# Kernel optimization log

Hardware: AMD Instinct MI355X
Metric: run time of the kernel (lower is better)

Reference implementation:

```python
import jax, jax.numpy as jnp
import numpy as np
import math

NUM_HEADS = 16


def setup_inputs() -> dict:
    key = jax.random.key(0)
    ks = jax.random.split(key, 5)
    B, C, H = 2, 2048, 1024
    return {
        "x": jax.random.normal(ks[0], (B, C, H), dtype=jnp.float32),
        "Wqkv_w": jax.random.normal(ks[1], (3 * H, H), dtype=jnp.float32) * (1.0 / math.sqrt(H)),
        "Wqkv_b": jax.random.normal(ks[2], (3 * H,), dtype=jnp.float32) * 0.02,
        "Wo_w": jax.random.normal(ks[3], (H, H), dtype=jnp.float32) * (1.0 / math.sqrt(H)),
        "Wo_b": jax.random.normal(ks[4], (H,), dtype=jnp.float32) * 0.02,
    }


def reference(x, Wqkv_w, Wqkv_b, Wo_w, Wo_b):
    B, C, H = x.shape
    nh = NUM_HEADS
    hd = H // nh
    # QKV projection (torch Linear: x @ W.T + b)
    qkv = x @ Wqkv_w.T + Wqkv_b                      # [B, C, 3H]
    qkv = qkv.reshape(B, C, 3, nh, hd)
    qkv = jnp.transpose(qkv, (2, 0, 3, 1, 4))        # [3, B, nh, C, hd]
    q, k, v = qkv[0], qkv[1], qkv[2]
    scale = 1.0 / math.sqrt(hd)
    att = jnp.einsum('bhqd,bhkd->bhqk', q, k) * scale  # [B, nh, C, C]
    causal = jnp.triu(jnp.ones((C, C), dtype=bool), k=1)  # True above diagonal
    att = jnp.where(causal[None, None], jnp.float32(-jnp.inf), att)
    att = jax.nn.softmax(att, axis=-1)
    # dropout p set to 0 (eval-mode math)
    out = jnp.einsum('bhqk,bhkd->bhqd', att, v)       # [B, nh, C, hd]
    out = jnp.transpose(out, (0, 2, 1, 3)).reshape(B, C, H)
    return out @ Wo_w.T + Wo_b
```

## Files before the change

### kernel.cpp

```cpp
#include <hip/hip_runtime.h>
#include <hip/hip_bf16.h>
#include <math.h>

typedef unsigned short u16;
typedef __attribute__((ext_vector_type(8))) __bf16 bf16x8;
typedef __attribute__((ext_vector_type(4))) float f32x4;
typedef __attribute__((ext_vector_type(8))) unsigned short u16x8;
typedef __attribute__((ext_vector_type(4))) unsigned int u32x4;

__device__ __forceinline__ u16 f2bf(float f) {
  union { float f; unsigned u; } x; x.f = f;
  unsigned r = x.u + 0x7fffu + ((x.u >> 16) & 1u);
  return (u16)(r >> 16);
}

__device__ __forceinline__ void gload16(const u16* g, u16* l) {
  __builtin_amdgcn_global_load_lds(
      (const __attribute__((address_space(1))) void*)g,
      (__attribute__((address_space(3))) void*)l, 16, 0, 0);
}

#define MFMA16(a, b, c) __builtin_amdgcn_mfma_f32_16x16x32_bf16((a), (b), (c), 0, 0, 0)

__global__ __launch_bounds__(256) void cast_bf16_kernel(
    const float* __restrict__ in, u16* __restrict__ out, int n4) {
  int i = blockIdx.x * 256 + threadIdx.x;
  if (i >= n4) return;
  f32x4 v = *(const f32x4*)(in + (size_t)i * 4);
  u16 o0 = f2bf(v[0]), o1 = f2bf(v[1]), o2 = f2bf(v[2]), o3 = f2bf(v[3]);
  unsigned lo = (unsigned)o0 | ((unsigned)o1 << 16);
  unsigned hi = (unsigned)o2 | ((unsigned)o3 << 16);
  ((unsigned*)out)[(size_t)i * 2] = lo;
  ((unsigned*)out)[(size_t)i * 2 + 1] = hi;
}

__device__ __forceinline__ void gemm_bt_128(
    const u16* __restrict__ A, const u16* __restrict__ B, int K, int m0, int n0,
    u16* As, u16* Bs, f32x4 acc[4][4]) {
  const int tid = threadIdx.x;
  const int lane = tid & 63;
  const int wr = tid >> 7;
  const int wc = (tid >> 6) & 1;
  for (int k0 = 0; k0 < K; k0 += 64) {
    #pragma unroll
    for (int it = 0; it < 4; ++it) {
      int c = it * 256 + tid;
      int row = c >> 3;
      int ko = (c & 7) << 3;
      gload16(A + (size_t)(m0 + row) * K + (k0 + ko), As + c * 8);
      gload16(B + (size_t)(n0 + row) * K + (k0 + ko), Bs + c * 8);
    }
    __syncthreads();
    #pragma unroll
    for (int kk = 0; kk < 2; ++kk) {
      bf16x8 a[4], b[4];
      #pragma unroll
      for (int m = 0; m < 4; ++m)
        a[m] = *(const bf16x8*)(As + ((wr * 64 + m * 16 + (lane & 15)) * 64 +
                                      kk * 32 + ((lane >> 4) << 3)));
      #pragma unroll
      for (int n = 0; n < 4; ++n)
        b[n] = *(const bf16x8*)(Bs + ((wc * 64 + n * 16 + (lane & 15)) * 64 +
                                      kk * 32 + ((lane >> 4) << 3)));
      #pragma unroll
      for (int m = 0; m < 4; ++m)
        #pragma unroll
        for (int n = 0; n < 4; ++n)
          acc[m][n] = MFMA16(a[m], b[n], acc[m][n]);
    }
    __syncthreads();
  }
}

__global__ __launch_bounds__(256) void gemm_qkv_kernel(
    const u16* __restrict__ X, const u16* __restrict__ W, const float* __restrict__ bias,
    u16* __restrict__ Qb, u16* __restrict__ Kb, u16* __restrict__ Vb) {
  __shared__ __align__(16) u16 As[128 * 64];
  __shared__ __align__(16) u16 Bs[128 * 64];
  f32x4 acc[4][4];
  #pragma unroll
  for (int m = 0; m < 4; ++m)
    #pragma unroll
    for (int n = 0; n < 4; ++n) acc[m][n] = (f32x4){0.f, 0.f, 0.f, 0.f};
  const int m0 = blockIdx.y * 128;
  const int n0 = blockIdx.x * 128;
  gemm_bt_128(X, W, 1024, m0, n0, As, Bs, acc);
  const int lane = threadIdx.x & 63;
  const int wr = threadIdx.x >> 7, wc = (threadIdx.x >> 6) & 1;
  #pragma unroll
  for (int m = 0; m < 4; ++m) {
    #pragma unroll
    for (int n = 0; n < 4; ++n) {
      #pragma unroll
      for (int j = 0; j < 4; ++j) {
        int row = m0 + wr * 64 + m * 16 + ((lane >> 4) << 2) + j;
        int col = n0 + wc * 64 + n * 16 + (lane & 15);
        float v = acc[m][n][j] + bias[col];
        int which = col >> 10;
        int rem = col & 1023;
        int h = rem >> 6, d = rem & 63;
        int bb = row >> 11, q = row & 2047;
        if (which == 0) v *= 0.125f;
        u16* dst = (which == 0) ? Qb : (which == 1 ? Kb : Vb);
        dst[((size_t)((bb * 16 + h) * 2048 + q)) * 64 + d] = f2bf(v);
      }
    }
  }
}

__global__ __launch_bounds__(256) void gemm_out_kernel(
    const u16* __restrict__ Ain, const u16* __restrict__ W, const float* __restrict__ bias,
    float* __restrict__ out) {
  __shared__ __align__(16) u16 As[128 * 64];
  __shared__ __align__(16) u16 Bs[128 * 64];
  f32x4 acc[4][4];
  #pragma unroll
  for (int m = 0; m < 4; ++m)
    #pragma unroll
    for (int n = 0; n < 4; ++n) acc[m][n] = (f32x4){0.f, 0.f, 0.f, 0.f};
  const int m0 = blockIdx.y * 128;
  const int n0 = blockIdx.x * 128;
  gemm_bt_128(Ain, W, 1024, m0, n0, As, Bs, acc);
  const int lane = threadIdx.x & 63;
  const int wr = threadIdx.x >> 7, wc = (threadIdx.x >> 6) & 1;
  #pragma unroll
  for (int m = 0; m < 4; ++m) {
    #pragma unroll
    for (int n = 0; n < 4; ++n) {
      #pragma unroll
      for (int j = 0; j < 4; ++j) {
        int row = m0 + wr * 64 + m * 16 + ((lane >> 4) << 2) + j;
        int col = n0 + wc * 64 + n * 16 + (lane & 15);
        out[(size_t)row * 1024 + col] = acc[m][n][j] + bias[col];
      }
    }
  }
}

__device__ __forceinline__ void attn_one(
    const u16* __restrict__ Qh, const u16* __restrict__ Kh, const u16* __restrict__ Vh,
    u16* __restrict__ Ob, int bb, int h, int qt,
    u16 (*Ks)[64 * 64], u16 (*Vt)[64 * 64]) {
  const int tid = threadIdx.x, lane = tid & 63, w = tid >> 6;
  const int g = lane >> 4, q15 = lane & 15;

  bf16x8 qf[2];
  const int qrow = qt * 64 + w * 16 + q15;
  #pragma unroll
  for (int kk = 0; kk < 2; ++kk)
    qf[kk] = *(const bf16x8*)(Qh + (size_t)qrow * 64 + kk * 32 + g * 8);

  f32x4 acc_o[4];
  #pragma unroll
  for (int n = 0; n < 4; ++n) acc_o[n] = (f32x4){0.f, 0.f, 0.f, 0.f};
  float m_run = -INFINITY, l_run = 0.f;

  const int nt = qt + 1;

  auto stageK = [&](int t, int buf) {
    #pragma unroll
    for (int it = 0; it < 2; ++it) {
      int c = it * 256 + tid;
      int row = c >> 3, b8 = c & 7;
      gload16(Kh + (size_t)(t * 64 + row) * 64 + ((b8 ^ (row & 7)) << 3),
              Ks[buf] + c * 8);
    }
  };

  stageK(0, 0);
  #pragma unroll
  for (int it = 0; it < 2; ++it) {
    int kloc = it * 32 + (tid >> 3);
    int d0 = (tid & 7) << 3;
    u16x8 v = *(const u16x8*)(Vh + (size_t)kloc * 64 + d0);
    #pragma unroll
    for (int i = 0; i < 8; ++i) {
      int d = d0 + i;
      int fv = (d + (d >> 3)) & 7;
      Vt[0][d * 64 + (((kloc >> 3) ^ fv) << 3) + (kloc & 7)] = v[i];
    }
  }
  __syncthreads();

  for (int t = 0; t < nt; ++t) {
    const int cur = t & 1;
    const bool pre = (t + 1 < nt);
    u16x8 vreg[2];
    if (pre) {
      stageK(t + 1, cur ^ 1);
      #pragma unroll
      for (int it = 0; it < 2; ++it) {
        int kloc = it * 32 + (tid >> 3);
        int d0 = (tid & 7) << 3;
        vreg[it] = *(const u16x8*)(Vh + (size_t)((t + 1) * 64 + kloc) * 64 + d0);
      }
    }

    f32x4 accs[4];
    __builtin_amdgcn_s_setprio(1);
    #pragma unroll
    for (int cb = 0; cb < 4; ++cb) {
      accs[cb] = (f32x4){0.f, 0.f, 0.f, 0.f};
      #pragma unroll
      for (int kk = 0; kk < 2; ++kk) {
        int row = cb * 16 + q15;
        int kblk = kk * 4 + g;
        bf16x8 kf = *(const bf16x8*)(Ks[cur] + row * 64 + ((kblk ^ (row & 7)) << 3));
        accs[cb] = MFMA16(kf, qf[kk], accs[cb]);
      }
    }
    __builtin_amdgcn_s_setprio(0);
    if (t == nt - 1) {
      #pragma unroll
      for (int cb = 0; cb < 4; ++cb)
        #pragma unroll
        for (int j = 0; j < 4; ++j) {
          int kg = t * 64 + cb * 16 + 4 * g + j;
          int qg = qt * 64 + w * 16 + q15;
          if (kg > qg) accs[cb][j] = -INFINITY;
        }
    }

    float mj = accs[0][0];
    #pragma unroll
    for (int cb = 0; cb < 4; ++cb)
      #pragma unroll
      for (int j = 0; j < 4; ++j) mj = fmaxf(mj, accs[cb][j]);
    mj = fmaxf(mj, __shfl_xor(mj, 16));
    mj = fmaxf(mj, __shfl_xor(mj, 32));
    float mn = fmaxf(m_run, mj);
    float sc = __expf(m_run - mn);
    m_run = mn;
    float rs = 0.f;
    #pragma unroll
    for (int cb = 0; cb < 4; ++cb)
      #pragma unroll
      for (int j = 0; j < 4; ++j) {
        float p = __expf(accs[cb][j] - mn);
        accs[cb][j] = p;
        rs += p;
      }
    rs += __shfl_xor(rs, 16);
    rs += __shfl_xor(rs, 32);
    l_run = l_run * sc + rs;

    float scj[4];
    #pragma unroll
    for (int j = 0; j < 4; ++j) scj[j] = __shfl(sc, 4 * g + j);
    #pragma unroll
    for (int n = 0; n < 4; ++n)
      #pragma unroll
      for (int j = 0; j < 4; ++j) acc_o[n][j] *= scj[j];

    unsigned Wp[4][2];
    #pragma unroll
    for (int cb = 0; cb < 4; ++cb)
      #pragma unroll
      for (int hh = 0; hh < 2; ++hh)
        asm("v_cvt_pk_bf16_f32 %0, %1, %2"
            : "=v"(Wp[cb][hh]) : "v"(accs[cb][2 * hh]), "v"(accs[cb][2 * hh + 1]));

    unsigned aw[2][4];
    #pragma unroll
    for (int kk = 0; kk < 2; ++kk)
      #pragma unroll
      for (int iw = 0; iw < 4; ++iw) {
        int srcLane = q15 + ((((g & 1) << 1) + (iw >> 1)) << 4);
        unsigned c0 = __shfl(Wp[2 * kk + 0][iw & 1], srcLane);
        unsigned c1 = __shfl(Wp[2 * kk + 1][iw & 1], srcLane);
        aw[kk][iw] = (g >> 1) ? c1 : c0;
      }
    bf16x8 pa0 = __builtin_bit_cast(bf16x8, (u32x4){aw[0][0], aw[0][1], aw[0][2], aw[0][3]});
    bf16x8 pa1 = __builtin_bit_cast(bf16x8, (u32x4){aw[1][0], aw[1][1], aw[1][2], aw[1][3]});

    __builtin_amdgcn_s_setprio(1);
    #pragma unroll
    for (int n = 0; n < 4; ++n) {
      #pragma unroll
      for (int kk = 0; kk < 2; ++kk) {
        int cblk = kk * 4 + g;
        int d = n * 16 + q15;
        int fv = (d + (d >> 3)) & 7;
        bf16x8 vb = *(const bf16x8*)(Vt[cur] + d * 64 + ((cblk ^ fv) << 3));
        acc_o[n] = MFMA16(kk ? pa1 : pa0, vb, acc_o[n]);
      }
    }
    __builtin_amdgcn_s_setprio(0);

    if (pre) {
      #pragma unroll
      for (int it = 0; it < 2; ++it) {
        int kloc = it * 32 + (tid >> 3);
        int d0 = (tid & 7) << 3;
        #pragma unroll
        for (int i = 0; i < 8; ++i) {
          int d = d0 + i;
          int fv = (d + (d >> 3)) & 7;
          Vt[cur ^ 1][d * 64 + (((kloc >> 3) ^ fv) << 3) + (kloc & 7)] = vreg[it][i];
        }
      }
    }
    __syncthreads();
  }

  float invl = 1.0f / l_run;
  float invj[4];
  #pragma unroll
  for (int j = 0; j < 4; ++j) invj[j] = __shfl(invl, 4 * g + j);
  #pragma unroll
  for (int n = 0; n < 4; ++n)
    #pragma unroll
    for (int j = 0; j < 4; ++j) {
      int qg = qt * 64 + w * 16 + 4 * g + j;
      Ob[((size_t)(bb * 2048 + qg)) * 1024 + h * 64 + n * 16 + q15] =
          f2bf(acc_o[n][j] * invj[j]);
    }
}

__global__ __launch_bounds__(256, 4) void attn_kernel(
    const u16* __restrict__ Qb, const u16* __restrict__ Kb, const u16* __restrict__ Vb,
    u16* __restrict__ Ob) {
  __shared__ __align__(16) u16 Ks[2][64 * 64];
  __shared__ __align__(16) u16 Vt[2][64 * 64];
  const int blk = blockIdx.x;
  const int p = blk & 15;
  const int bh = blk >> 4;
  const size_t base = (size_t)bh * 2048 * 64;
  const int bb = bh >> 4, h = bh & 15;
  attn_one(Qb + base, Kb + base, Vb + base, Ob, bb, h, 31 - p, Ks, Vt);
  attn_one(Qb + base, Kb + base, Vb + base, Ob, bb, h, p, Ks, Vt);
}

extern "C" void kernel_launch(void* const* d_in, const int* in_sizes, int n_in,
                              void* d_out, int out_size, void* d_ws, size_t ws_size,
                              hipStream_t stream) {
  const float* x    = (const float*)d_in[0];
  const float* wqkv = (const float*)d_in[1];
  const float* bqkv = (const float*)d_in[2];
  const float* wo   = (const float*)d_in[3];
  const float* bo   = (const float*)d_in[4];
  float* out = (float*)d_out;

  const size_t MB = 1u << 20;
  char* ws = (char*)d_ws;
  u16* x_bf  = (u16*)(ws);
  u16* wq_bf = (u16*)(ws + 8 * MB);
  u16* wo_bf = (u16*)(ws + 14 * MB);
  u16* q_buf = (u16*)(ws + 16 * MB);
  u16* k_buf = (u16*)(ws + 24 * MB);
  u16* v_buf = (u16*)(ws + 32 * MB);
  u16* a_out = (u16*)(ws + 40 * MB);

  cast_bf16_kernel<<<4096, 256, 0, stream>>>(x, x_bf, 1048576);
  cast_bf16_kernel<<<3072, 256, 0, stream>>>(wqkv, wq_bf, 786432);
  cast_bf16_kernel<<<1024, 256, 0, stream>>>(wo, wo_bf, 262144);

  gemm_qkv_kernel<<<dim3(24, 32), 256, 0, stream>>>(x_bf, wq_bf, bqkv,
                                                    q_buf, k_buf, v_buf);
  attn_kernel<<<512, 256, 0, stream>>>(q_buf, k_buf, v_buf, a_out);
  gemm_out_kernel<<<dim3(8, 32), 256, 0, stream>>>(a_out, wo_bf, bo, out);
}
```

Before: 153.4 us.

## Rework attention with 32x32 MFMA, pre-transposed V from QKV GEMM, exp2 softmax

The QKV GEMM epilogue now writes V already transposed (head, d, seq) and folds log2(e)/sqrt(hd) into Q, so softmax can use exp2f. The attention kernel switches to 128-thread blocks with 2 waves, each owning 32 query rows and using 32x32x16 MFMAs. K and V tiles are both staged into LDS with async global_load_lds instead of a register round-trip and scalar transposed stores. This removes the per-tile V transpose and most cross-lane shuffles. In exchange there are fewer waves per block, higher register pressure, and strided transposed stores in the GEMM epilogue.

```diff
diff --git a/kernel.cpp b/kernel.cpp
--- a/kernel.cpp
+++ b/kernel.cpp
@@ -5,8 +5,10 @@
 typedef unsigned short u16;
 typedef __attribute__((ext_vector_type(8))) __bf16 bf16x8;
 typedef __attribute__((ext_vector_type(4))) float f32x4;
+typedef __attribute__((ext_vector_type(16))) float f32x16;
 typedef __attribute__((ext_vector_type(8))) unsigned short u16x8;
 typedef __attribute__((ext_vector_type(4))) unsigned int u32x4;
+typedef __attribute__((ext_vector_type(2))) unsigned int u32x2;
 
 __device__ __forceinline__ u16 f2bf(float f) {
   union { float f; unsigned u; } x; x.f = f;
@@ -21,6 +23,9 @@
 }
 
 #define MFMA16(a, b, c) __builtin_amdgcn_mfma_f32_16x16x32_bf16((a), (b), (c), 0, 0, 0)
+#define MFMA32(a, b, c) __builtin_amdgcn_mfma_f32_32x32x16_bf16((a), (b), (c), 0, 0, 0)
+
+#define QSCALE 0.18033688011112043f
 
 __global__ __launch_bounds__(256) void cast_bf16_kernel(
     const float* __restrict__ in, u16* __restrict__ out, int n4) {
@@ -74,7 +79,7 @@
 
 __global__ __launch_bounds__(256) void gemm_qkv_kernel(
     const u16* __restrict__ X, const u16* __restrict__ W, const float* __restrict__ bias,
-    u16* __restrict__ Qb, u16* __restrict__ Kb, u16* __restrict__ Vb) {
+    u16* __restrict__ Qb, u16* __restrict__ Kb, u16* __restrict__ VTb) {
   __shared__ __align__(16) u16 As[128 * 64];
   __shared__ __align__(16) u16 Bs[128 * 64];
   f32x4 acc[4][4];
@@ -100,9 +105,14 @@
         int rem = col & 1023;
         int h = rem >> 6, d = rem & 63;
         int bb = row >> 11, q = row & 2047;
-        if (which == 0) v *= 0.125f;
-        u16* dst = (which == 0) ? Qb : (which == 1 ? Kb : Vb);
-        dst[((size_t)((bb * 16 + h) * 2048 + q)) * 64 + d] = f2bf(v);
+        int hh = bb * 16 + h;
+        if (which == 0) {
+          Qb[((size_t)hh * 2048 + q) * 64 + d] = f2bf(v * QSCALE);
+        } else if (which == 1) {
+          Kb[((size_t)hh * 2048 + q) * 64 + d] = f2bf(v);
+        } else {
+          VTb[((size_t)hh * 64 + d) * 2048 + q] = f2bf(v);
+        }
       }
     }
   }
@@ -138,187 +148,150 @@
 }
 
 __device__ __forceinline__ void attn_one(
-    const u16* __restrict__ Qh, const u16* __restrict__ Kh, const u16* __restrict__ Vh,
-    u16* __restrict__ Ob, int bb, int h, int qt,
+    const u16* __restrict__ Qh, const u16* __restrict__ Kh, const u16* __restrict__ VTh,
+    u16* __restrict__ Ob, int bb, int h, int qb,
     u16 (*Ks)[64 * 64], u16 (*Vt)[64 * 64]) {
   const int tid = threadIdx.x, lane = tid & 63, w = tid >> 6;
-  const int g = lane >> 4, q15 = lane & 15;
-
-  bf16x8 qf[2];
-  const int qrow = qt * 64 + w * 16 + q15;
-  #pragma unroll
-  for (int kk = 0; kk < 2; ++kk)
-    qf[kk] = *(const bf16x8*)(Qh + (size_t)qrow * 64 + kk * 32 + g * 8);
-
-  f32x4 acc_o[4];
-  #pragma unroll
-  for (int n = 0; n < 4; ++n) acc_o[n] = (f32x4){0.f, 0.f, 0.f, 0.f};
+  const int half = lane >> 5, q31 = lane & 31;
+  const int qrow = qb * 64 + w * 32 + q31;
+
+  bf16x8 qf[4];
+  #pragma unroll
+  for (int ds = 0; ds < 4; ++ds)
+    qf[ds] = *(const bf16x8*)(Qh + (size_t)qrow * 64 + ds * 16 + half * 8);
+
+  f32x16 acc_o[2] = {};
   float m_run = -INFINITY, l_run = 0.f;
-
-  const int nt = qt + 1;
+  const int nt = qb + 1;
 
   auto stageK = [&](int t, int buf) {
     #pragma unroll
-    for (int it = 0; it < 2; ++it) {
-      int c = it * 256 + tid;
+    for (int it = 0; it < 4; ++it) {
+      int c = it * 128 + tid;
       int row = c >> 3, b8 = c & 7;
       gload16(Kh + (size_t)(t * 64 + row) * 64 + ((b8 ^ (row & 7)) << 3),
               Ks[buf] + c * 8);
     }
   };
+  auto stageV = [&](int t, int buf) {
+    #pragma unroll
+    for (int it = 0; it < 4; ++it) {
+      int c = it * 128 + tid;
+      int d = c >> 3, b8 = c & 7;
+      int fv = (d + (d >> 3)) & 7;
+      gload16(VTh + (size_t)d * 2048 + t * 64 + ((b8 ^ fv) << 3),
+              Vt[buf] + c * 8);
+    }
+  };
 
   stageK(0, 0);
-  #pragma unroll
-  for (int it = 0; it < 2; ++it) {
-    int kloc = it * 32 + (tid >> 3);
-    int d0 = (tid & 7) << 3;
-    u16x8 v = *(const u16x8*)(Vh + (size_t)kloc * 64 + d0);
-    #pragma unroll
-    for (int i = 0; i < 8; ++i) {
-      int d = d0 + i;
-      int fv = (d + (d >> 3)) & 7;
-      Vt[0][d * 64 + (((kloc >> 3) ^ fv) << 3) + (kloc & 7)] = v[i];
-    }
-  }
+  stageV(0, 0);
   __syncthreads();
 
   for (int t = 0; t < nt; ++t) {
     const int cur = t & 1;
-    const bool pre = (t + 1 < nt);
-    u16x8 vreg[2];
-    if (pre) {
-      stageK(t + 1, cur ^ 1);
-      #pragma unroll
-      for (int it = 0; it < 2; ++it) {
-        int kloc = it * 32 + (tid >> 3);
-        int d0 = (tid & 7) << 3;
-        vreg[it] = *(const u16x8*)(Vh + (size_t)((t + 1) * 64 + kloc) * 64 + d0);
-      }
-    }
-
-    f32x4 accs[4];
+    if (t + 1 < nt) { stageK(t + 1, cur ^ 1); stageV(t + 1, cur ^ 1); }
+
+    f32x16 accs[2] = {};
     __builtin_amdgcn_s_setprio(1);
     #pragma unroll
-    for (int cb = 0; cb < 4; ++cb) {
-      accs[cb] = (f32x4){0.f, 0.f, 0.f, 0.f};
-      #pragma unroll
-      for (int kk = 0; kk < 2; ++kk) {
-        int row = cb * 16 + q15;
-        int kblk = kk * 4 + g;
-        bf16x8 kf = *(const bf16x8*)(Ks[cur] + row * 64 + ((kblk ^ (row & 7)) << 3));
-        accs[cb] = MFMA16(kf, qf[kk], accs[cb]);
+    for (int c = 0; c < 2; ++c) {
+      #pragma unroll
+      for (int ds = 0; ds < 4; ++ds) {
+        int row = c * 32 + q31;
+        int bi = 2 * ds + half;
+        bf16x8 kf = *(const bf16x8*)(Ks[cur] + row * 64 + ((bi ^ (row & 7)) << 3));
+        accs[c] = MFMA32(kf, qf[ds], accs[c]);
       }
     }
     __builtin_amdgcn_s_setprio(0);
+
     if (t == nt - 1) {
       #pragma unroll
-      for (int cb = 0; cb < 4; ++cb)
+      for (int c = 0; c < 2; ++c)
         #pragma unroll
-        for (int j = 0; j < 4; ++j) {
-          int kg = t * 64 + cb * 16 + 4 * g + j;
-          int qg = qt * 64 + w * 16 + q15;
-          if (kg > qg) accs[cb][j] = -INFINITY;
+        for (int r = 0; r < 16; ++r) {
+          int kg = t * 64 + c * 32 + (r & 3) + 8 * (r >> 2) + 4 * half;
+          if (kg > qrow) accs[c][r] = -INFINITY;
         }
     }
 
     float mj = accs[0][0];
     #pragma unroll
-    for (int cb = 0; cb < 4; ++cb)
-      #pragma unroll
-      for (int j = 0; j < 4; ++j) mj = fmaxf(mj, accs[cb][j]);
-    mj = fmaxf(mj, __shfl_xor(mj, 16));
+    for (int c = 0; c < 2; ++c)
+      #pragma unroll
+      for (int r = 0; r < 16; ++r) mj = fmaxf(mj, accs[c][r]);
     mj = fmaxf(mj, __shfl_xor(mj, 32));
     float mn = fmaxf(m_run, mj);
-    float sc = __expf(m_run - mn);
+    float sc = exp2f(m_run - mn);
     m_run = mn;
     float rs = 0.f;
     #pragma unroll
-    for (int cb = 0; cb < 4; ++cb)
-      #pragma unroll
-      for (int j = 0; j < 4; ++j) {
-        float p = __expf(accs[cb][j] - mn);
-        accs[cb][j] = p;
+    for (int c = 0; c < 2; ++c)
+      #pragma unroll
+      for (int r = 0; r < 16; ++r) {
+        float p = exp2f(accs[c][r] - mn);
+        accs[c][r] = p;
         rs += p;
       }
-    rs += __shfl_xor(rs, 16);
     rs += __shfl_xor(rs, 32);
     l_run = l_run * sc + rs;
-
-    float scj[4];
-    #pragma unroll
-    for (int j = 0; j < 4; ++j) scj[j] = __shfl(sc, 4 * g + j);
-    #pragma unroll
-    for (int n = 0; n < 4; ++n)
-      #pragma unroll
-      for (int j = 0; j < 4; ++j) acc_o[n][j] *= scj[j];
-
-    unsigned Wp[4][2];
-    #pragma unroll
-    for (int cb = 0; cb < 4; ++cb)
-      #pragma unroll
-      for (int hh = 0; hh < 2; ++hh)
+    acc_o[0] *= sc;
+    acc_o[1] *= sc;
+
+    unsigned Wp[2][8];
+    #pragma unroll
+    for (int c = 0; c < 2; ++c)
+      #pragma unroll
+      for (int m = 0; m < 8; ++m)
         asm("v_cvt_pk_bf16_f32 %0, %1, %2"
-            : "=v"(Wp[cb][hh]) : "v"(accs[cb][2 * hh]), "v"(accs[cb][2 * hh + 1]));
-
-    unsigned aw[2][4];
-    #pragma unroll
-    for (int kk = 0; kk < 2; ++kk)
-      #pragma unroll
-      for (int iw = 0; iw < 4; ++iw) {
-        int srcLane = q15 + ((((g & 1) << 1) + (iw >> 1)) << 4);
-        unsigned c0 = __shfl(Wp[2 * kk + 0][iw & 1], srcLane);
-        unsigned c1 = __shfl(Wp[2 * kk + 1][iw & 1], srcLane);
-        aw[kk][iw] = (g >> 1) ? c1 : c0;
-      }
-    bf16x8 pa0 = __builtin_bit_cast(bf16x8, (u32x4){aw[0][0], aw[0][1], aw[0][2], aw[0][3]});
-    bf16x8 pa1 = __builtin_bit_cast(bf16x8, (u32x4){aw[1][0], aw[1][1], aw[1][2], aw[1][3]});
-
-    __builtin_amdgcn_s_setprio(1);
-    #pragma unroll
-    for (int n = 0; n < 4; ++n) {
-      #pragma unroll
-      for (int kk = 0; kk < 2; ++kk) {
-        int cblk = kk * 4 + g;
-        int d = n * 16 + q15;
+            : "=v"(Wp[c][m]) : "v"(accs[c][2 * m]), "v"(accs[c][2 * m + 1]));
+
+    #pragma unroll
+    for (int k = 0; k < 4; ++k) {
+      const int c = k >> 1, g0 = 4 * (k & 1);
+      unsigned x0 = (unsigned)__shfl_xor((int)Wp[c][g0 + 0], 32);
+      unsigned x1 = (unsigned)__shfl_xor((int)Wp[c][g0 + 1], 32);
+      unsigned x2 = (unsigned)__shfl_xor((int)Wp[c][g0 + 2], 32);
+      unsigned x3 = (unsigned)__shfl_xor((int)Wp[c][g0 + 3], 32);
+      unsigned pa0 = half ? x2 : Wp[c][g0 + 0];
+      unsigned pa1 = half ? x3 : Wp[c][g0 + 1];
+      unsigned pa2 = half ? Wp[c][g0 + 2] : x0;
+      unsigned pa3 = half ? Wp[c][g0 + 3] : x1;
+      bf16x8 pb = __builtin_bit_cast(bf16x8, (u32x4){pa0, pa1, pa2, pa3});
+      __builtin_amdgcn_s_setprio(1);
+      #pragma unroll
+      for (int n = 0; n < 2; ++n) {
+        int d = n * 32 + q31;
         int fv = (d + (d >> 3)) & 7;
-        bf16x8 vb = *(const bf16x8*)(Vt[cur] + d * 64 + ((cblk ^ fv) << 3));
-        acc_o[n] = MFMA16(kk ? pa1 : pa0, vb, acc_o[n]);
-      }
-    }
-    __builtin_amdgcn_s_setprio(0);
-
-    if (pre) {
-      #pragma unroll
-      for (int it = 0; it < 2; ++it) {
-        int kloc = it * 32 + (tid >> 3);
-        int d0 = (tid & 7) << 3;
-        #pragma unroll
-        for (int i = 0; i < 8; ++i) {
-          int d = d0 + i;
-          int fv = (d + (d >> 3)) & 7;
-          Vt[cur ^ 1][d * 64 + (((kloc >> 3) ^ fv) << 3) + (kloc & 7)] = vreg[it][i];
-        }
-      }
+        int bi = 2 * k + half;
+        bf16x8 vf = *(const bf16x8*)(Vt[cur] + d * 64 + ((bi ^ fv) << 3));
+        acc_o[n] = MFMA32(vf, pb, acc_o[n]);
+      }
+      __builtin_amdgcn_s_setprio(0);
     }
     __syncthreads();
   }
 
   float invl = 1.0f / l_run;
-  float invj[4];
-  #pragma unroll
-  for (int j = 0; j < 4; ++j) invj[j] = __shfl(invl, 4 * g + j);
-  #pragma unroll
-  for (int n = 0; n < 4; ++n)
-    #pragma unroll
-    for (int j = 0; j < 4; ++j) {
-      int qg = qt * 64 + w * 16 + 4 * g + j;
-      Ob[((size_t)(bb * 2048 + qg)) * 1024 + h * 64 + n * 16 + q15] =
-          f2bf(acc_o[n][j] * invj[j]);
-    }
-}
-
-__global__ __launch_bounds__(256, 4) void attn_kernel(
-    const u16* __restrict__ Qb, const u16* __restrict__ Kb, const u16* __restrict__ Vb,
+  #pragma unroll
+  for (int n = 0; n < 2; ++n)
+    #pragma unroll
+    for (int rq = 0; rq < 4; ++rq) {
+      int dbase = n * 32 + 8 * rq + 4 * half;
+      u16 o0 = f2bf(acc_o[n][4 * rq + 0] * invl);
+      u16 o1 = f2bf(acc_o[n][4 * rq + 1] * invl);
+      u16 o2 = f2bf(acc_o[n][4 * rq + 2] * invl);
+      u16 o3 = f2bf(acc_o[n][4 * rq + 3] * invl);
+      unsigned lo = (unsigned)o0 | ((unsigned)o1 << 16);
+      unsigned hi = (unsigned)o2 | ((unsigned)o3 << 16);
+      size_t idx = ((size_t)(bb * 2048 + qrow)) * 1024 + h * 64 + dbase;
+      *(u32x2*)(Ob + idx) = (u32x2){lo, hi};
+    }
+}
+
+__global__ __launch_bounds__(128, 2) void attn_kernel(
+    const u16* __restrict__ Qb, const u16* __restrict__ Kb, const u16* __restrict__ VTb,
     u16* __restrict__ Ob) {
   __shared__ __align__(16) u16 Ks[2][64 * 64];
   __shared__ __align__(16) u16 Vt[2][64 * 64];
@@ -327,8 +300,8 @@
   const int bh = blk >> 4;
   const size_t base = (size_t)bh * 2048 * 64;
   const int bb = bh >> 4, h = bh & 15;
-  attn_one(Qb + base, Kb + base, Vb + base, Ob, bb, h, 31 - p, Ks, Vt);
-  attn_one(Qb + base, Kb + base, Vb + base, Ob, bb, h, p, Ks, Vt);
+  attn_one(Qb + base, Kb + base, VTb + base, Ob, bb, h, 31 - p, Ks, Vt);
+  attn_one(Qb + base, Kb + base, VTb + base, Ob, bb, h, p, Ks, Vt);
 }
 
 extern "C" void kernel_launch(void* const* d_in, const int* in_sizes, int n_in,
@@ -348,7 +321,7 @@
   u16* wo_bf = (u16*)(ws + 14 * MB);
   u16* q_buf = (u16*)(ws + 16 * MB);
   u16* k_buf = (u16*)(ws + 24 * MB);
-  u16* v_buf = (u16*)(ws + 32 * MB);
+  u16* vt_buf= (u16*)(ws + 32 * MB);
   u16* a_out = (u16*)(ws + 40 * MB);
 
   cast_bf16_kernel<<<4096, 256, 0, stream>>>(x, x_bf, 1048576);
@@ -356,7 +329,7 @@
   cast_bf16_kernel<<<1024, 256, 0, stream>>>(wo, wo_bf, 262144);
 
   gemm_qkv_kernel<<<dim3(24, 32), 256, 0, stream>>>(x_bf, wq_bf, bqkv,
-                                                    q_buf, k_buf, v_buf);
-  attn_kernel<<<512, 256, 0, stream>>>(q_buf, k_buf, v_buf, a_out);
+                                                    q_buf, k_buf, vt_buf);
+  attn_kernel<<<512, 128, 0, stream>>>(q_buf, k_buf, vt_buf, a_out);
   gemm_out_kernel<<<dim3(8, 32), 256, 0, stream>>>(a_out, wo_bf, bo, out);
 }
```

New measurement: 186.7 us. 21.7% more time.

## Store V transposed, stage it via async LDS loads, add persistent atomic work queue

Applied to the files above, without the earlier changes.

The QKV GEMM now writes V pre-transposed, so attention can stage V tiles with asynchronous global-to-LDS loads instead of register loads followed by scattered LDS stores. Q is pre-scaled by log2(e)/sqrt(d) so the softmax uses exp2f. The attention kernel becomes persistent, pulling work units from an atomic counter ordered longest-first, with occupancy lowered to 3 blocks per CU and a 768-block grid. The counter lives in the last word of the output buffer and is reset by the QKV GEMM. That slot is later overwritten by the out-projection, but this depends on kernel ordering, and the transposed V stores are strided (uncoalesced) writes.

```diff
diff --git a/kernel.cpp b/kernel.cpp
--- a/kernel.cpp
+++ b/kernel.cpp
@@ -21,6 +21,8 @@
 }
 
 #define MFMA16(a, b, c) __builtin_amdgcn_mfma_f32_16x16x32_bf16((a), (b), (c), 0, 0, 0)
+
+#define QSCALE 0.18033688011112043f
 
 __global__ __launch_bounds__(256) void cast_bf16_kernel(
     const float* __restrict__ in, u16* __restrict__ out, int n4) {
@@ -74,7 +76,9 @@
 
 __global__ __launch_bounds__(256) void gemm_qkv_kernel(
     const u16* __restrict__ X, const u16* __restrict__ W, const float* __restrict__ bias,
-    u16* __restrict__ Qb, u16* __restrict__ Kb, u16* __restrict__ Vb) {
+    u16* __restrict__ Qb, u16* __restrict__ Kb, u16* __restrict__ VTb,
+    unsigned* __restrict__ cnt) {
+  if (threadIdx.x == 0 && blockIdx.x == 0 && blockIdx.y == 0) *cnt = 0u;
   __shared__ __align__(16) u16 As[128 * 64];
   __shared__ __align__(16) u16 Bs[128 * 64];
   f32x4 acc[4][4];
@@ -100,9 +104,14 @@
         int rem = col & 1023;
         int h = rem >> 6, d = rem & 63;
         int bb = row >> 11, q = row & 2047;
-        if (which == 0) v *= 0.125f;
-        u16* dst = (which == 0) ? Qb : (which == 1 ? Kb : Vb);
-        dst[((size_t)((bb * 16 + h) * 2048 + q)) * 64 + d] = f2bf(v);
+        int hh = bb * 16 + h;
+        if (which == 0) {
+          Qb[((size_t)hh * 2048 + q) * 64 + d] = f2bf(v * QSCALE);
+        } else if (which == 1) {
+          Kb[((size_t)hh * 2048 + q) * 64 + d] = f2bf(v);
+        } else {
+          VTb[((size_t)hh * 64 + d) * 2048 + q] = f2bf(v);
+        }
       }
     }
   }
@@ -138,7 +147,7 @@
 }
 
 __device__ __forceinline__ void attn_one(
-    const u16* __restrict__ Qh, const u16* __restrict__ Kh, const u16* __restrict__ Vh,
+    const u16* __restrict__ Qh, const u16* __restrict__ Kh, const u16* __restrict__ VTh,
     u16* __restrict__ Ob, int bb, int h, int qt,
     u16 (*Ks)[64 * 64], u16 (*Vt)[64 * 64]) {
   const int tid = threadIdx.x, lane = tid & 63, w = tid >> 6;
@@ -166,35 +175,24 @@
               Ks[buf] + c * 8);
     }
   };
+  auto stageV = [&](int t, int buf) {
+    #pragma unroll
+    for (int it = 0; it < 2; ++it) {
+      int c = it * 256 + tid;
+      int d = c >> 3, b8 = c & 7;
+      int fv = (d + (d >> 3)) & 7;
+      gload16(VTh + (size_t)d * 2048 + t * 64 + ((b8 ^ fv) << 3),
+              Vt[buf] + c * 8);
+    }
+  };
 
   stageK(0, 0);
-  #pragma unroll
-  for (int it = 0; it < 2; ++it) {
-    int kloc = it * 32 + (tid >> 3);
-    int d0 = (tid & 7) << 3;
-    u16x8 v = *(const u16x8*)(Vh + (size_t)kloc * 64 + d0);
-    #pragma unroll
-    for (int i = 0; i < 8; ++i) {
-      int d = d0 + i;
-      int fv = (d + (d >> 3)) & 7;
-      Vt[0][d * 64 + (((kloc >> 3) ^ fv) << 3) + (kloc & 7)] = v[i];
-    }
-  }
+  stageV(0, 0);
   __syncthreads();
 
   for (int t = 0; t < nt; ++t) {
     const int cur = t & 1;
-    const bool pre = (t + 1 < nt);
-    u16x8 vreg[2];
-    if (pre) {
-      stageK(t + 1, cur ^ 1);
-      #pragma unroll
-      for (int it = 0; it < 2; ++it) {
-        int kloc = it * 32 + (tid >> 3);
-        int d0 = (tid & 7) << 3;
-        vreg[it] = *(const u16x8*)(Vh + (size_t)((t + 1) * 64 + kloc) * 64 + d0);
-      }
-    }
+    if (t + 1 < nt) { stageK(t + 1, cur ^ 1); stageV(t + 1, cur ^ 1); }
 
     f32x4 accs[4];
     __builtin_amdgcn_s_setprio(1);
@@ -216,8 +214,7 @@
         #pragma unroll
         for (int j = 0; j < 4; ++j) {
           int kg = t * 64 + cb * 16 + 4 * g + j;
-          int qg = qt * 64 + w * 16 + q15;
-          if (kg > qg) accs[cb][j] = -INFINITY;
+          if (kg > qrow) accs[cb][j] = -INFINITY;
         }
     }
 
@@ -229,14 +226,14 @@
     mj = fmaxf(mj, __shfl_xor(mj, 16));
     mj = fmaxf(mj, __shfl_xor(mj, 32));
     float mn = fmaxf(m_run, mj);
-    float sc = __expf(m_run - mn);
+    float sc = exp2f(m_run - mn);
     m_run = mn;
     float rs = 0.f;
     #pragma unroll
     for (int cb = 0; cb < 4; ++cb)
       #pragma unroll
       for (int j = 0; j < 4; ++j) {
-        float p = __expf(accs[cb][j] - mn);
+        float p = exp2f(accs[cb][j] - mn);
         accs[cb][j] = p;
         rs += p;
       }
@@ -286,20 +283,6 @@
       }
     }
     __builtin_amdgcn_s_setprio(0);
-
-    if (pre) {
-      #pragma unroll
-      for (int it = 0; it < 2; ++it) {
-        int kloc = it * 32 + (tid >> 3);
-        int d0 = (tid & 7) << 3;
-        #pragma unroll
-        for (int i = 0; i < 8; ++i) {
-          int d = d0 + i;
-          int fv = (d + (d >> 3)) & 7;
-          Vt[cur ^ 1][d * 64 + (((kloc >> 3) ^ fv) << 3) + (kloc & 7)] = vreg[it][i];
-        }
-      }
-    }
     __syncthreads();
   }
 
@@ -317,18 +300,23 @@
     }
 }
 
-__global__ __launch_bounds__(256, 4) void attn_kernel(
-    const u16* __restrict__ Qb, const u16* __restrict__ Kb, const u16* __restrict__ Vb,
-    u16* __restrict__ Ob) {
+__global__ __launch_bounds__(256, 3) void attn_kernel(
+    const u16* __restrict__ Qb, const u16* __restrict__ Kb, const u16* __restrict__ VTb,
+    u16* __restrict__ Ob, unsigned* __restrict__ cnt) {
   __shared__ __align__(16) u16 Ks[2][64 * 64];
   __shared__ __align__(16) u16 Vt[2][64 * 64];
-  const int blk = blockIdx.x;
-  const int p = blk & 15;
-  const int bh = blk >> 4;
-  const size_t base = (size_t)bh * 2048 * 64;
-  const int bb = bh >> 4, h = bh & 15;
-  attn_one(Qb + base, Kb + base, Vb + base, Ob, bb, h, 31 - p, Ks, Vt);
-  attn_one(Qb + base, Kb + base, Vb + base, Ob, bb, h, p, Ks, Vt);
+  __shared__ unsigned s_unit;
+  for (;;) {
+    if (threadIdx.x == 0) s_unit = atomicAdd(cnt, 1u);
+    __syncthreads();
+    unsigned u = s_unit;
+    if (u >= 1024u) return;
+    const int qt = 31 - (int)(u >> 5);
+    const int bh = (int)(u & 31u);
+    const size_t base = (size_t)bh * 2048 * 64;
+    attn_one(Qb + base, Kb + base, VTb + base, Ob, bh >> 4, bh & 15, qt, Ks, Vt);
+    __syncthreads();
+  }
 }
 
 extern "C" void kernel_launch(void* const* d_in, const int* in_sizes, int n_in,
@@ -348,15 +336,17 @@
   u16* wo_bf = (u16*)(ws + 14 * MB);
   u16* q_buf = (u16*)(ws + 16 * MB);
   u16* k_buf = (u16*)(ws + 24 * MB);
-  u16* v_buf = (u16*)(ws + 32 * MB);
+  u16* vt_buf= (u16*)(ws + 32 * MB);
   u16* a_out = (u16*)(ws + 40 * MB);
+
+  unsigned* cnt = (unsigned*)((char*)d_out + (size_t)out_size * 4 - 4);
 
   cast_bf16_kernel<<<4096, 256, 0, stream>>>(x, x_bf, 1048576);
   cast_bf16_kernel<<<3072, 256, 0, stream>>>(wqkv, wq_bf, 786432);
   cast_bf16_kernel<<<1024, 256, 0, stream>>>(wo, wo_bf, 262144);
 
   gemm_qkv_kernel<<<dim3(24, 32), 256, 0, stream>>>(x_bf, wq_bf, bqkv,
-                                                    q_buf, k_buf, v_buf);
-  attn_kernel<<<512, 256, 0, stream>>>(q_buf, k_buf, v_buf, a_out);
+                                                    q_buf, k_buf, vt_buf, cnt);
+  attn_kernel<<<768, 256, 0, stream>>>(q_buf, k_buf, vt_buf, a_out, cnt);
   gemm_out_kernel<<<dim3(8, 32), 256, 0, stream>>>(a_out, wo_bf, bo, out);
 }
```

After: 168.2 us. 9.7% more time.
